# Kernel tuning notes

Hardware: AMD Instinct MI355X
Metric: run time of the kernel (lower is better)

## Reference

```python
import jax, jax.numpy as jnp
import numpy as np

LP_NORM = 1.2  # Lp_norm init kwarg


def setup_inputs() -> dict:
    key = jax.random.key(0)
    k0, k1, k2, k3 = jax.random.split(key, 4)
    B, L, D, H, K = 16, 1024, 512, 256, 4
    bound = np.sqrt(6.0) / np.sqrt(2.0 * H)
    x = jax.random.normal(k0, (B, L, D), dtype=jnp.float32)
    # A_selector: nn.Linear(embed_size, num_A) -> weight (K, D), bias (K,)
    W_sel = jax.random.normal(k1, (K, D), dtype=jnp.float32) * 0.02
    b_sel = jnp.zeros((K,), dtype=jnp.float32)
    # B: nn.Linear(embed_size, hidden_size, bias=False) -> weight (H, D)
    W_B = jax.random.normal(k2, (H, D), dtype=jnp.float32) * 0.02
    # A_dict: uniform in [-sqrt(6)/sqrt(2H), +sqrt(6)/sqrt(2H)], shape (H, H, K)
    A_dict = jax.random.uniform(k3, (H, H, K), dtype=jnp.float32,
                                minval=-bound, maxval=bound)
    return {"x": x, "W_sel": W_sel, "b_sel": b_sel, "W_B": W_B, "A_dict": A_dict}


def reference(x, W_sel, b_sel, W_B, A_dict):
    B, L, D = x.shape
    H = A_dict.shape[0]
    # selections = softmax(A_selector(x))  -> (B, L, K)
    sel = jax.nn.softmax(jnp.einsum('bld,kd->blk', x, W_sel) + b_sel, axis=-1)
    # inputs_ = B(x) -> (B, L, H)
    inputs_ = jnp.einsum('bld,hd->blh', x, W_B)

    def step(h, xs):
        s_t, u_t = xs  # (B, K), (B, H)
        # mix transition matrices: (H, H, K) x (B, K) -> (B, H, H)
        A = jnp.einsum('ijk,bk->bij', A_dict, s_t)
        # Lp norm over dim=1 (rows, n1), normalize columns
        norm = jnp.sum(jnp.abs(A) ** LP_NORM, axis=1) ** (1.0 / LP_NORM)  # (B, H)
        A = A / norm[:, None, :]
        h_new = jnp.einsum('bij,bj->bi', A, h) + u_t
        return h_new, h_new

    h0 = jnp.zeros((B, H), dtype=x.dtype)
    sel_t = jnp.swapaxes(sel, 0, 1)       # (L, B, K)
    inp_t = jnp.swapaxes(inputs_, 0, 1)   # (L, B, H)
    _, ys = jax.lax.scan(step, h0, (sel_t, inp_t))  # ys: (L, B, H)
    return jnp.swapaxes(ys, 0, 1)  # (B, L, H)
```

## Files before the change

kernel.cpp:

```cpp
#include <hip/hip_runtime.h>

#define B_DIM 16
#define L_DIM 1024
#define D_DIM 512
#define H_DIM 256
#define K_DIM 4

#define SLICES 8
#define RPW 32

#define OFF_HB  0
#define OFF_SEL 65536
#define OFF_RN  327680

__device__ __forceinline__ float fast_log2(float x) { return __builtin_amdgcn_logf(x); }
__device__ __forceinline__ float fast_exp2(float x) { return __builtin_amdgcn_exp2f(x); }

__global__ void k_init(unsigned long long* hb) {
    int tid = blockIdx.x * blockDim.x + threadIdx.x;
    for (int i = tid; i < 2 * 16 * 256; i += 512) hb[i] = 0ull;
}

__global__ __launch_bounds__(256) void k_sel(const float* __restrict__ x,
                                             const float* __restrict__ Wsel,
                                             const float* __restrict__ bsel,
                                             float* __restrict__ SEL) {
    int row  = blockIdx.x * 4 + (threadIdx.x >> 6);
    int lane = threadIdx.x & 63;
    const float4* x4 = (const float4*)(x + (size_t)row * D_DIM);
    const float4* w4 = (const float4*)Wsel;
    float4 xa = x4[lane * 2], xb = x4[lane * 2 + 1];
    float acc[4];
#pragma unroll
    for (int k = 0; k < 4; ++k) {
        float4 wa = w4[k * (D_DIM / 4) + lane * 2];
        float4 wb = w4[k * (D_DIM / 4) + lane * 2 + 1];
        acc[k] = xa.x * wa.x + xa.y * wa.y + xa.z * wa.z + xa.w * wa.w +
                 xb.x * wb.x + xb.y * wb.y + xb.z * wb.z + xb.w * wb.w;
    }
#pragma unroll
    for (int off = 1; off < 64; off <<= 1) {
#pragma unroll
        for (int k = 0; k < 4; ++k) acc[k] += __shfl_xor(acc[k], off, 64);
    }
    if (lane == 0) {
        float z[4], mx = -1e30f;
#pragma unroll
        for (int k = 0; k < 4; ++k) { z[k] = acc[k] + bsel[k]; mx = fmaxf(mx, z[k]); }
        float e[4], s = 0.0f;
#pragma unroll
        for (int k = 0; k < 4; ++k) { e[k] = fast_exp2((z[k] - mx) * 1.4426950408889634f); s += e[k]; }
        float inv = 1.0f / s;
        float4 o = { e[0] * inv, e[1] * inv, e[2] * inv, e[3] * inv };
        ((float4*)SEL)[row] = o;
    }
}

#define GBM 64
#define GBN 64
#define GBK 32
__global__ __launch_bounds__(256) void k_u(const float* __restrict__ X,
                                           const float* __restrict__ W,
                                           float* __restrict__ U) {
    __shared__ float Xs[GBK][GBM + 1];
    __shared__ float Ws[GBK][GBN + 1];
    int tid = threadIdx.x;
    int rb = blockIdx.y * GBM;
    int cb = blockIdx.x * GBN;
    int tr = tid >> 4, tc = tid & 15;
    int lrow = tid >> 2;
    int lcol = (tid & 3) * 8;
    float acc[4][4] = {};
    for (int kt = 0; kt < D_DIM; kt += GBK) {
        float4 xa = *(const float4*)(X + (size_t)(rb + lrow) * D_DIM + kt + lcol);
        float4 xb = *(const float4*)(X + (size_t)(rb + lrow) * D_DIM + kt + lcol + 4);
        float4 wa = *(const float4*)(W + (size_t)(cb + lrow) * D_DIM + kt + lcol);
        float4 wb = *(const float4*)(W + (size_t)(cb + lrow) * D_DIM + kt + lcol + 4);
        __syncthreads();
        Xs[lcol + 0][lrow] = xa.x; Xs[lcol + 1][lrow] = xa.y;
        Xs[lcol + 2][lrow] = xa.z; Xs[lcol + 3][lrow] = xa.w;
        Xs[lcol + 4][lrow] = xb.x; Xs[lcol + 5][lrow] = xb.y;
        Xs[lcol + 6][lrow] = xb.z; Xs[lcol + 7][lrow] = xb.w;
        Ws[lcol + 0][lrow] = wa.x; Ws[lcol + 1][lrow] = wa.y;
        Ws[lcol + 2][lrow] = wa.z; Ws[lcol + 3][lrow] = wa.w;
        Ws[lcol + 4][lrow] = wb.x; Ws[lcol + 5][lrow] = wb.y;
        Ws[lcol + 6][lrow] = wb.z; Ws[lcol + 7][lrow] = wb.w;
        __syncthreads();
#pragma unroll
        for (int kk = 0; kk < GBK; ++kk) {
            float a0 = Xs[kk][tr * 4 + 0], a1 = Xs[kk][tr * 4 + 1];
            float a2 = Xs[kk][tr * 4 + 2], a3 = Xs[kk][tr * 4 + 3];
            float b0 = Ws[kk][tc * 4 + 0], b1 = Ws[kk][tc * 4 + 1];
            float b2 = Ws[kk][tc * 4 + 2], b3 = Ws[kk][tc * 4 + 3];
            acc[0][0] = fmaf(a0, b0, acc[0][0]); acc[0][1] = fmaf(a0, b1, acc[0][1]);
            acc[0][2] = fmaf(a0, b2, acc[0][2]); acc[0][3] = fmaf(a0, b3, acc[0][3]);
            acc[1][0] = fmaf(a1, b0, acc[1][0]); acc[1][1] = fmaf(a1, b1, acc[1][1]);
            acc[1][2] = fmaf(a1, b2, acc[1][2]); acc[1][3] = fmaf(a1, b3, acc[1][3]);
            acc[2][0] = fmaf(a2, b0, acc[2][0]); acc[2][1] = fmaf(a2, b1, acc[2][1]);
            acc[2][2] = fmaf(a2, b2, acc[2][2]); acc[2][3] = fmaf(a2, b3, acc[2][3]);
            acc[3][0] = fmaf(a3, b0, acc[3][0]); acc[3][1] = fmaf(a3, b1, acc[3][1]);
            acc[3][2] = fmaf(a3, b2, acc[3][2]); acc[3][3] = fmaf(a3, b3, acc[3][3]);
        }
        __syncthreads();
    }
#pragma unroll
    for (int mi = 0; mi < 4; ++mi) {
        float4 v = { acc[mi][0], acc[mi][1], acc[mi][2], acc[mi][3] };
        *(float4*)(U + (size_t)(rb + tr * 4 + mi) * H_DIM + cb + tc * 4) = v;
    }
}

__global__ __launch_bounds__(256) void k_norm(const float* __restrict__ M,
                                              const float* __restrict__ SEL,
                                              float* __restrict__ rN) {
    int wg = blockIdx.x;
    int b = wg >> 6;
    int t0 = (wg & 63) << 4;
    int j = threadIdx.x;
    float s[16][4];
#pragma unroll
    for (int tt = 0; tt < 16; ++tt) {
        float4 sv = ((const float4*)SEL)[b * L_DIM + t0 + tt];
        s[tt][0] = sv.x; s[tt][1] = sv.y; s[tt][2] = sv.z; s[tt][3] = sv.w;
    }
    float acc[16] = {};
    const float4* M4 = (const float4*)M;
    for (int i = 0; i < H_DIM; ++i) {
        float4 m = M4[i * H_DIM + j];
#pragma unroll
        for (int tt = 0; tt < 16; ++tt) {
            float a = fmaf(m.x, s[tt][0], fmaf(m.y, s[tt][1],
                      fmaf(m.z, s[tt][2], m.w * s[tt][3])));
            a = fabsf(a);
            acc[tt] += fast_exp2(1.2f * fast_log2(a));
        }
    }
#pragma unroll
    for (int tt = 0; tt < 16; ++tt) {
        rN[(size_t)(b * L_DIM + t0 + tt) * H_DIM + j] =
            fast_exp2(-0.8333333333f * fast_log2(acc[tt]));
    }
}

__global__ __launch_bounds__(256, 1) void k_scan(const float* __restrict__ M,
                                                 const float* __restrict__ SEL,
                                                 const float* __restrict__ rN,
                                                 float* __restrict__ out,
                                                 unsigned long long* hb) {
    const int wg = blockIdx.x;
    const int b = wg & 15;
    const int slice = wg >> 4;
    const int tid = threadIdx.x;
    const int q = tid >> 6;
    const int ti = tid & 63;
    const int r = ti & 31;
    const int js = ti >> 5;
    const int ig = slice * RPW + r;
    const int jbase = q * 64 + js * 32;

    float m[128];
    {
        const float4* M4 = (const float4*)M;
#pragma unroll
        for (int jj = 0; jj < 32; ++jj) {
            float4 v = M4[ig * H_DIM + jbase + jj];
            m[jj * 4 + 0] = v.x; m[jj * 4 + 1] = v.y;
            m[jj * 4 + 2] = v.z; m[jj * 4 + 3] = v.w;
        }
    }

    __shared__ float g_lds[256];
    __shared__ float part_lds[256];

#pragma unroll 1
    for (int t = 0; t < L_DIM; ++t) {
        float rn = rN[(size_t)(b * L_DIM + t) * H_DIM + tid];
        float4 s4 = ((const float4*)SEL)[b * L_DIM + t];
        float uval = 0.0f;
        if (tid < RPW) uval = out[(size_t)(b * L_DIM + t) * H_DIM + slice * RPW + tid];

        unsigned long long* src = hb + (size_t)(t & 1) * (16 * 256) + b * 256 + tid;
        unsigned long long w;
        while (((w = __hip_atomic_load(src, __ATOMIC_RELAXED, __HIP_MEMORY_SCOPE_AGENT)) >> 32)
               != (unsigned int)t)
            __builtin_amdgcn_s_sleep(1);
        float h = __uint_as_float((unsigned int)w);
        g_lds[tid] = h * rn;
        __syncthreads();

        float acc0 = 0, acc1 = 0, acc2 = 0, acc3 = 0;
        const float4* g4 = (const float4*)(g_lds + jbase);
#pragma unroll
        for (int jj4 = 0; jj4 < 8; ++jj4) {
            float4 gv = g4[jj4];
            acc0 = fmaf(m[(jj4 * 4 + 0) * 4 + 0], gv.x, acc0);
            acc1 = fmaf(m[(jj4 * 4 + 0) * 4 + 1], gv.x, acc1);
            acc2 = fmaf(m[(jj4 * 4 + 0) * 4 + 2], gv.x, acc2);
            acc3 = fmaf(m[(jj4 * 4 + 0) * 4 + 3], gv.x, acc3);
            acc0 = fmaf(m[(jj4 * 4 + 1) * 4 + 0], gv.y, acc0);
            acc1 = fmaf(m[(jj4 * 4 + 1) * 4 + 1], gv.y, acc1);
            acc2 = fmaf(m[(jj4 * 4 + 1) * 4 + 2], gv.y, acc2);
            acc3 = fmaf(m[(jj4 * 4 + 1) * 4 + 3], gv.y, acc3);
            acc0 = fmaf(m[(jj4 * 4 + 2) * 4 + 0], gv.z, acc0);
            acc1 = fmaf(m[(jj4 * 4 + 2) * 4 + 1], gv.z, acc1);
            acc2 = fmaf(m[(jj4 * 4 + 2) * 4 + 2], gv.z, acc2);
            acc3 = fmaf(m[(jj4 * 4 + 2) * 4 + 3], gv.z, acc3);
            acc0 = fmaf(m[(jj4 * 4 + 3) * 4 + 0], gv.w, acc0);
            acc1 = fmaf(m[(jj4 * 4 + 3) * 4 + 1], gv.w, acc1);
            acc2 = fmaf(m[(jj4 * 4 + 3) * 4 + 2], gv.w, acc2);
            acc3 = fmaf(m[(jj4 * 4 + 3) * 4 + 3], gv.w, acc3);
        }
        float part = fmaf(acc0, s4.x, fmaf(acc1, s4.y, fmaf(acc2, s4.z, acc3 * s4.w)));
        part_lds[tid] = part;
        __syncthreads();

        if (tid < RPW) {
            float hn = uval;
#pragma unroll
            for (int p = 0; p < 8; ++p) hn += part_lds[tid + 32 * p];
            out[(size_t)(b * L_DIM + t) * H_DIM + slice * RPW + tid] = hn;
            unsigned long long pw = ((unsigned long long)(unsigned int)(t + 1) << 32) |
                                    (unsigned long long)__float_as_uint(hn);
            __hip_atomic_store(hb + (size_t)((t + 1) & 1) * (16 * 256) + b * 256 + slice * RPW + tid,
                               pw, __ATOMIC_RELAXED, __HIP_MEMORY_SCOPE_AGENT);
        }
    }
}

extern "C" void kernel_launch(void* const* d_in, const int* in_sizes, int n_in,
                              void* d_out, int out_size, void* d_ws, size_t ws_size,
                              hipStream_t stream) {
    const float* x    = (const float*)d_in[0];
    const float* Wsel = (const float*)d_in[1];
    const float* bsel = (const float*)d_in[2];
    const float* W_B  = (const float*)d_in[3];
    const float* M    = (const float*)d_in[4];
    float* out = (float*)d_out;

    char* ws = (char*)d_ws;
    unsigned long long* hb = (unsigned long long*)(ws + OFF_HB);
    float* SEL = (float*)(ws + OFF_SEL);
    float* rN  = (float*)(ws + OFF_RN);

    k_init<<<1, 512, 0, stream>>>(hb);
    k_sel<<<(B_DIM * L_DIM) / 4, 256, 0, stream>>>(x, Wsel, bsel, SEL);
    k_u<<<dim3(H_DIM / GBN, (B_DIM * L_DIM) / GBM), 256, 0, stream>>>(x, W_B, out);
    k_norm<<<(B_DIM * L_DIM) / 16, 256, 0, stream>>>(M, SEL, rN);
    k_scan<<<B_DIM * SLICES, 256, 0, stream>>>(M, SEL, rN, out, hb);
}
```

Before: 1.368 ms.

## Remap scan threads so row reduction uses wave shuffles, dropping one barrier

```diff
diff --git a/kernel.cpp b/kernel.cpp
--- a/kernel.cpp
+++ b/kernel.cpp
@@ -152,32 +152,31 @@
     const int slice = wg >> 4;
     const int tid = threadIdx.x;
     const int q = tid >> 6;
-    const int ti = tid & 63;
-    const int r = ti & 31;
-    const int js = ti >> 5;
-    const int ig = slice * RPW + r;
-    const int jbase = q * 64 + js * 32;
+    const int lane = tid & 63;
+    const int ro = lane & 7;
+    const int chunk = lane >> 3;
+    const int row = slice * RPW + q * 8 + ro;
+    const int jbase = chunk * 32;
 
     float m[128];
     {
         const float4* M4 = (const float4*)M;
 #pragma unroll
         for (int jj = 0; jj < 32; ++jj) {
-            float4 v = M4[ig * H_DIM + jbase + jj];
+            float4 v = M4[row * H_DIM + jbase + jj];
             m[jj * 4 + 0] = v.x; m[jj * 4 + 1] = v.y;
             m[jj * 4 + 2] = v.z; m[jj * 4 + 3] = v.w;
         }
     }
 
-    __shared__ float g_lds[256];
-    __shared__ float part_lds[256];
+    __shared__ float g_lds[2][256];
 
 #pragma unroll 1
     for (int t = 0; t < L_DIM; ++t) {
         float rn = rN[(size_t)(b * L_DIM + t) * H_DIM + tid];
         float4 s4 = ((const float4*)SEL)[b * L_DIM + t];
         float uval = 0.0f;
-        if (tid < RPW) uval = out[(size_t)(b * L_DIM + t) * H_DIM + slice * RPW + tid];
+        if (lane < 8) uval = out[(size_t)(b * L_DIM + t) * H_DIM + row];
 
         unsigned long long* src = hb + (size_t)(t & 1) * (16 * 256) + b * 256 + tid;
         unsigned long long w;
@@ -185,11 +184,11 @@
                != (unsigned int)t)
             __builtin_amdgcn_s_sleep(1);
         float h = __uint_as_float((unsigned int)w);
-        g_lds[tid] = h * rn;
+        g_lds[t & 1][tid] = h * rn;
         __syncthreads();
 
         float acc0 = 0, acc1 = 0, acc2 = 0, acc3 = 0;
-        const float4* g4 = (const float4*)(g_lds + jbase);
+        const float4* g4 = (const float4*)(&g_lds[t & 1][jbase]);
 #pragma unroll
         for (int jj4 = 0; jj4 < 8; ++jj4) {
             float4 gv = g4[jj4];
@@ -211,18 +210,17 @@
             acc3 = fmaf(m[(jj4 * 4 + 3) * 4 + 3], gv.w, acc3);
         }
         float part = fmaf(acc0, s4.x, fmaf(acc1, s4.y, fmaf(acc2, s4.z, acc3 * s4.w)));
-        part_lds[tid] = part;
-        __syncthreads();
-
-        if (tid < RPW) {
-            float hn = uval;
-#pragma unroll
-            for (int p = 0; p < 8; ++p) hn += part_lds[tid + 32 * p];
-            out[(size_t)(b * L_DIM + t) * H_DIM + slice * RPW + tid] = hn;
+        part += __shfl_xor(part, 8, 64);
+        part += __shfl_xor(part, 16, 64);
+        part += __shfl_xor(part, 32, 64);
+
+        if (lane < 8) {
+            float hn = part + uval;
             unsigned long long pw = ((unsigned long long)(unsigned int)(t + 1) << 32) |
                                     (unsigned long long)__float_as_uint(hn);
-            __hip_atomic_store(hb + (size_t)((t + 1) & 1) * (16 * 256) + b * 256 + slice * RPW + tid,
+            __hip_atomic_store(hb + (size_t)((t + 1) & 1) * (16 * 256) + b * 256 + row,
                                pw, __ATOMIC_RELAXED, __HIP_MEMORY_SCOPE_AGENT);
+            out[(size_t)(b * L_DIM + t) * H_DIM + row] = hn;
         }
     }
 }
```

Measured after the change: 1.568 ms. +14.7%, slower.

## Fuse selector softmax, norm and input GEMM into one heterogeneous kernel

Applied to the files above, without the earlier changes.

```diff
diff --git a/kernel.cpp b/kernel.cpp
--- a/kernel.cpp
+++ b/kernel.cpp
@@ -21,124 +21,132 @@
     for (int i = tid; i < 2 * 16 * 256; i += 512) hb[i] = 0ull;
 }
 
-__global__ __launch_bounds__(256) void k_sel(const float* __restrict__ x,
-                                             const float* __restrict__ Wsel,
-                                             const float* __restrict__ bsel,
-                                             float* __restrict__ SEL) {
-    int row  = blockIdx.x * 4 + (threadIdx.x >> 6);
-    int lane = threadIdx.x & 63;
-    const float4* x4 = (const float4*)(x + (size_t)row * D_DIM);
-    const float4* w4 = (const float4*)Wsel;
-    float4 xa = x4[lane * 2], xb = x4[lane * 2 + 1];
-    float acc[4];
-#pragma unroll
-    for (int k = 0; k < 4; ++k) {
-        float4 wa = w4[k * (D_DIM / 4) + lane * 2];
-        float4 wb = w4[k * (D_DIM / 4) + lane * 2 + 1];
-        acc[k] = xa.x * wa.x + xa.y * wa.y + xa.z * wa.z + xa.w * wa.w +
-                 xb.x * wb.x + xb.y * wb.y + xb.z * wb.z + xb.w * wb.w;
-    }
-#pragma unroll
-    for (int off = 1; off < 64; off <<= 1) {
-#pragma unroll
-        for (int k = 0; k < 4; ++k) acc[k] += __shfl_xor(acc[k], off, 64);
-    }
-    if (lane == 0) {
-        float z[4], mx = -1e30f;
-#pragma unroll
-        for (int k = 0; k < 4; ++k) { z[k] = acc[k] + bsel[k]; mx = fmaxf(mx, z[k]); }
-        float e[4], s = 0.0f;
-#pragma unroll
-        for (int k = 0; k < 4; ++k) { e[k] = fast_exp2((z[k] - mx) * 1.4426950408889634f); s += e[k]; }
-        float inv = 1.0f / s;
-        float4 o = { e[0] * inv, e[1] * inv, e[2] * inv, e[3] * inv };
-        ((float4*)SEL)[row] = o;
-    }
-}
-
 #define GBM 64
 #define GBN 64
 #define GBK 32
-__global__ __launch_bounds__(256) void k_u(const float* __restrict__ X,
-                                           const float* __restrict__ W,
-                                           float* __restrict__ U) {
+__global__ __launch_bounds__(256) void k_par(const float* __restrict__ x,
+                                             const float* __restrict__ Wsel,
+                                             const float* __restrict__ bsel,
+                                             const float* __restrict__ W_B,
+                                             const float* __restrict__ M,
+                                             float* __restrict__ SEL,
+                                             float* __restrict__ rN,
+                                             float* __restrict__ out) {
     __shared__ float Xs[GBK][GBM + 1];
     __shared__ float Ws[GBK][GBN + 1];
-    int tid = threadIdx.x;
-    int rb = blockIdx.y * GBM;
-    int cb = blockIdx.x * GBN;
-    int tr = tid >> 4, tc = tid & 15;
-    int lrow = tid >> 2;
-    int lcol = (tid & 3) * 8;
-    float acc[4][4] = {};
-    for (int kt = 0; kt < D_DIM; kt += GBK) {
-        float4 xa = *(const float4*)(X + (size_t)(rb + lrow) * D_DIM + kt + lcol);
-        float4 xb = *(const float4*)(X + (size_t)(rb + lrow) * D_DIM + kt + lcol + 4);
-        float4 wa = *(const float4*)(W + (size_t)(cb + lrow) * D_DIM + kt + lcol);
-        float4 wb = *(const float4*)(W + (size_t)(cb + lrow) * D_DIM + kt + lcol + 4);
+    __shared__ float4 sel_lds[16];
+    const int bid = blockIdx.x;
+    const int tid = threadIdx.x;
+
+    if (bid < 1024) {
+        const int b = bid >> 6;
+        const int t0 = (bid & 63) << 4;
+        const int lane = tid & 63;
+        const int wv = tid >> 6;
+        const float4* w4 = (const float4*)Wsel;
+#pragma unroll
+        for (int rr = 0; rr < 4; ++rr) {
+            const int tt = wv * 4 + rr;
+            const int row = b * L_DIM + t0 + tt;
+            const float4* x4 = (const float4*)(x + (size_t)row * D_DIM);
+            float4 xa = x4[lane * 2], xb = x4[lane * 2 + 1];
+            float acc[4];
+#pragma unroll
+            for (int k = 0; k < 4; ++k) {
+                float4 wa = w4[k * (D_DIM / 4) + lane * 2];
+                float4 wb = w4[k * (D_DIM / 4) + lane * 2 + 1];
+                acc[k] = xa.x * wa.x + xa.y * wa.y + xa.z * wa.z + xa.w * wa.w +
+                         xb.x * wb.x + xb.y * wb.y + xb.z * wb.z + xb.w * wb.w;
+            }
+#pragma unroll
+            for (int off = 1; off < 64; off <<= 1) {
+#pragma unroll
+                for (int k = 0; k < 4; ++k) acc[k] += __shfl_xor(acc[k], off, 64);
+            }
+            if (lane == 0) {
+                float z[4], mx = -1e30f;
+#pragma unroll
+                for (int k = 0; k < 4; ++k) { z[k] = acc[k] + bsel[k]; mx = fmaxf(mx, z[k]); }
+                float e[4], s = 0.0f;
+#pragma unroll
+                for (int k = 0; k < 4; ++k) { e[k] = fast_exp2((z[k] - mx) * 1.4426950408889634f); s += e[k]; }
+                float inv = 1.0f / s;
+                float4 o = { e[0] * inv, e[1] * inv, e[2] * inv, e[3] * inv };
+                sel_lds[tt] = o;
+                ((float4*)SEL)[row] = o;
+            }
+        }
         __syncthreads();
-        Xs[lcol + 0][lrow] = xa.x; Xs[lcol + 1][lrow] = xa.y;
-        Xs[lcol + 2][lrow] = xa.z; Xs[lcol + 3][lrow] = xa.w;
-        Xs[lcol + 4][lrow] = xb.x; Xs[lcol + 5][lrow] = xb.y;
-        Xs[lcol + 6][lrow] = xb.z; Xs[lcol + 7][lrow] = xb.w;
-        Ws[lcol + 0][lrow] = wa.x; Ws[lcol + 1][lrow] = wa.y;
-        Ws[lcol + 2][lrow] = wa.z; Ws[lcol + 3][lrow] = wa.w;
-        Ws[lcol + 4][lrow] = wb.x; Ws[lcol + 5][lrow] = wb.y;
-        Ws[lcol + 6][lrow] = wb.z; Ws[lcol + 7][lrow] = wb.w;
-        __syncthreads();
-#pragma unroll
-        for (int kk = 0; kk < GBK; ++kk) {
-            float a0 = Xs[kk][tr * 4 + 0], a1 = Xs[kk][tr * 4 + 1];
-            float a2 = Xs[kk][tr * 4 + 2], a3 = Xs[kk][tr * 4 + 3];
-            float b0 = Ws[kk][tc * 4 + 0], b1 = Ws[kk][tc * 4 + 1];
-            float b2 = Ws[kk][tc * 4 + 2], b3 = Ws[kk][tc * 4 + 3];
-            acc[0][0] = fmaf(a0, b0, acc[0][0]); acc[0][1] = fmaf(a0, b1, acc[0][1]);
-            acc[0][2] = fmaf(a0, b2, acc[0][2]); acc[0][3] = fmaf(a0, b3, acc[0][3]);
-            acc[1][0] = fmaf(a1, b0, acc[1][0]); acc[1][1] = fmaf(a1, b1, acc[1][1]);
-            acc[1][2] = fmaf(a1, b2, acc[1][2]); acc[1][3] = fmaf(a1, b3, acc[1][3]);
-            acc[2][0] = fmaf(a2, b0, acc[2][0]); acc[2][1] = fmaf(a2, b1, acc[2][1]);
-            acc[2][2] = fmaf(a2, b2, acc[2][2]); acc[2][3] = fmaf(a2, b3, acc[2][3]);
-            acc[3][0] = fmaf(a3, b0, acc[3][0]); acc[3][1] = fmaf(a3, b1, acc[3][1]);
-            acc[3][2] = fmaf(a3, b2, acc[3][2]); acc[3][3] = fmaf(a3, b3, acc[3][3]);
-        }
-        __syncthreads();
-    }
-#pragma unroll
-    for (int mi = 0; mi < 4; ++mi) {
-        float4 v = { acc[mi][0], acc[mi][1], acc[mi][2], acc[mi][3] };
-        *(float4*)(U + (size_t)(rb + tr * 4 + mi) * H_DIM + cb + tc * 4) = v;
-    }
-}
-
-__global__ __launch_bounds__(256) void k_norm(const float* __restrict__ M,
-                                              const float* __restrict__ SEL,
-                                              float* __restrict__ rN) {
-    int wg = blockIdx.x;
-    int b = wg >> 6;
-    int t0 = (wg & 63) << 4;
-    int j = threadIdx.x;
-    float s[16][4];
-#pragma unroll
-    for (int tt = 0; tt < 16; ++tt) {
-        float4 sv = ((const float4*)SEL)[b * L_DIM + t0 + tt];
-        s[tt][0] = sv.x; s[tt][1] = sv.y; s[tt][2] = sv.z; s[tt][3] = sv.w;
-    }
-    float acc[16] = {};
-    const float4* M4 = (const float4*)M;
-    for (int i = 0; i < H_DIM; ++i) {
-        float4 m = M4[i * H_DIM + j];
+
+        const int j = tid;
+        float s[16][4];
 #pragma unroll
         for (int tt = 0; tt < 16; ++tt) {
-            float a = fmaf(m.x, s[tt][0], fmaf(m.y, s[tt][1],
-                      fmaf(m.z, s[tt][2], m.w * s[tt][3])));
-            a = fabsf(a);
-            acc[tt] += fast_exp2(1.2f * fast_log2(a));
-        }
-    }
-#pragma unroll
-    for (int tt = 0; tt < 16; ++tt) {
-        rN[(size_t)(b * L_DIM + t0 + tt) * H_DIM + j] =
-            fast_exp2(-0.8333333333f * fast_log2(acc[tt]));
+            float4 sv = sel_lds[tt];
+            s[tt][0] = sv.x; s[tt][1] = sv.y; s[tt][2] = sv.z; s[tt][3] = sv.w;
+        }
+        float acc[16] = {};
+        const float4* M4 = (const float4*)M;
+        for (int i = 0; i < H_DIM; ++i) {
+            float4 m = M4[i * H_DIM + j];
+#pragma unroll
+            for (int tt = 0; tt < 16; ++tt) {
+                float a = fmaf(m.x, s[tt][0], fmaf(m.y, s[tt][1],
+                          fmaf(m.z, s[tt][2], m.w * s[tt][3])));
+                a = fabsf(a);
+                acc[tt] += fast_exp2(1.2f * fast_log2(a));
+            }
+        }
+#pragma unroll
+        for (int tt = 0; tt < 16; ++tt) {
+            rN[(size_t)(b * L_DIM + t0 + tt) * H_DIM + j] =
+                fast_exp2(-0.8333333333f * fast_log2(acc[tt]));
+        }
+    } else {
+        const int w = bid - 1024;
+        const int cb = (w & 3) * GBN;
+        const int rb = (w >> 2) * GBM;
+        const int tr = tid >> 4, tc = tid & 15;
+        const int lrow = tid >> 2;
+        const int lcol = (tid & 3) * 8;
+        float acc[4][4] = {};
+        for (int kt = 0; kt < D_DIM; kt += GBK) {
+            float4 xa = *(const float4*)(x + (size_t)(rb + lrow) * D_DIM + kt + lcol);
+            float4 xb = *(const float4*)(x + (size_t)(rb + lrow) * D_DIM + kt + lcol + 4);
+            float4 wa = *(const float4*)(W_B + (size_t)(cb + lrow) * D_DIM + kt + lcol);
+            float4 wb = *(const float4*)(W_B + (size_t)(cb + lrow) * D_DIM + kt + lcol + 4);
+            __syncthreads();
+            Xs[lcol + 0][lrow] = xa.x; Xs[lcol + 1][lrow] = xa.y;
+            Xs[lcol + 2][lrow] = xa.z; Xs[lcol + 3][lrow] = xa.w;
+            Xs[lcol + 4][lrow] = xb.x; Xs[lcol + 5][lrow] = xb.y;
+            Xs[lcol + 6][lrow] = xb.z; Xs[lcol + 7][lrow] = xb.w;
+            Ws[lcol + 0][lrow] = wa.x; Ws[lcol + 1][lrow] = wa.y;
+            Ws[lcol + 2][lrow] = wa.z; Ws[lcol + 3][lrow] = wa.w;
+            Ws[lcol + 4][lrow] = wb.x; Ws[lcol + 5][lrow] = wb.y;
+            Ws[lcol + 6][lrow] = wb.z; Ws[lcol + 7][lrow] = wb.w;
+            __syncthreads();
+#pragma unroll
+            for (int kk = 0; kk < GBK; ++kk) {
+                float a0 = Xs[kk][tr * 4 + 0], a1 = Xs[kk][tr * 4 + 1];
+                float a2 = Xs[kk][tr * 4 + 2], a3 = Xs[kk][tr * 4 + 3];
+                float b0 = Ws[kk][tc * 4 + 0], b1 = Ws[kk][tc * 4 + 1];
+                float b2 = Ws[kk][tc * 4 + 2], b3 = Ws[kk][tc * 4 + 3];
+                acc[0][0] = fmaf(a0, b0, acc[0][0]); acc[0][1] = fmaf(a0, b1, acc[0][1]);
+                acc[0][2] = fmaf(a0, b2, acc[0][2]); acc[0][3] = fmaf(a0, b3, acc[0][3]);
+                acc[1][0] = fmaf(a1, b0, acc[1][0]); acc[1][1] = fmaf(a1, b1, acc[1][1]);
+                acc[1][2] = fmaf(a1, b2, acc[1][2]); acc[1][3] = fmaf(a1, b3, acc[1][3]);
+                acc[2][0] = fmaf(a2, b0, acc[2][0]); acc[2][1] = fmaf(a2, b1, acc[2][1]);
+                acc[2][2] = fmaf(a2, b2, acc[2][2]); acc[2][3] = fmaf(a2, b3, acc[2][3]);
+                acc[3][0] = fmaf(a3, b0, acc[3][0]); acc[3][1] = fmaf(a3, b1, acc[3][1]);
+                acc[3][2] = fmaf(a3, b2, acc[3][2]); acc[3][3] = fmaf(a3, b3, acc[3][3]);
+            }
+            __syncthreads();
+        }
+#pragma unroll
+        for (int mi = 0; mi < 4; ++mi) {
+            float4 v = { acc[mi][0], acc[mi][1], acc[mi][2], acc[mi][3] };
+            *(float4*)(out + (size_t)(rb + tr * 4 + mi) * H_DIM + cb + tc * 4) = v;
+        }
     }
 }
 
@@ -243,8 +251,6 @@
     float* rN  = (float*)(ws + OFF_RN);
 
     k_init<<<1, 512, 0, stream>>>(hb);
-    k_sel<<<(B_DIM * L_DIM) / 4, 256, 0, stream>>>(x, Wsel, bsel, SEL);
-    k_u<<<dim3(H_DIM / GBN, (B_DIM * L_DIM) / GBM), 256, 0, stream>>>(x, W_B, out);
-    k_norm<<<(B_DIM * L_DIM) / 16, 256, 0, stream>>>(M, SEL, rN);
+    k_par<<<2048, 256, 0, stream>>>(x, Wsel, bsel, W_B, M, SEL, rN, out);
     k_scan<<<B_DIM * SLICES, 256, 0, stream>>>(M, SEL, rN, out, hb);
 }
```

After: 1.326 ms. 3.1% less time.
